# Optimization experiments

Measured on AMD Instinct MI355X. Metric: run time of the kernel, lower is better.

Reference implementation:

```python
import jax, jax.numpy as jnp
import numpy as np
import math

D_MODEL = 1024
N_HEADS = 16
D_K = D_MODEL // N_HEADS
MAX_REL = 128


def setup_inputs() -> dict:
    key = jax.random.key(0)
    ks = jax.random.split(key, 10)
    B, S = 2, 2048
    std = 1.0 / math.sqrt(D_MODEL)
    inp = {
        "x": jax.random.normal(ks[0], (B, S, D_MODEL), dtype=jnp.float32),
        "Wq": jax.random.normal(ks[1], (D_MODEL, D_MODEL), dtype=jnp.float32) * std,
        "bq": jnp.zeros((D_MODEL,), dtype=jnp.float32),
        "Wk": jax.random.normal(ks[2], (D_MODEL, D_MODEL), dtype=jnp.float32) * std,
        "bk": jnp.zeros((D_MODEL,), dtype=jnp.float32),
        "Wv": jax.random.normal(ks[3], (D_MODEL, D_MODEL), dtype=jnp.float32) * std,
        "bv": jnp.zeros((D_MODEL,), dtype=jnp.float32),
        "Wo": jax.random.normal(ks[4], (D_MODEL, D_MODEL), dtype=jnp.float32) * std,
        "bo": jnp.zeros((D_MODEL,), dtype=jnp.float32),
        "rel_bias": jax.random.normal(ks[5], (N_HEADS, 2 * MAX_REL + 1), dtype=jnp.float32) * 0.02,
    }
    return inp


def _rel_bias_matrix(rel_bias, seq_len):
    # (H, S, S) gathered relative-position bias
    pos = jnp.arange(seq_len)
    rel = pos[:, None] - pos[None, :]
    idx = jnp.clip(rel, -MAX_REL, MAX_REL) + MAX_REL  # (S, S) in [0, 2M]
    return rel_bias[:, idx]  # (H, S, S)


def reference(x, Wq, bq, Wk, bk, Wv, bv, Wo, bo, rel_bias):
    B, S, _ = x.shape
    def proj(W, b):
        y = x @ W.T + b  # torch Linear: x @ W^T + b
        return y.reshape(B, S, N_HEADS, D_K).transpose(0, 2, 1, 3)  # (B,H,S,Dk)
    Q, K, V = proj(Wq, bq), proj(Wk, bk), proj(Wv, bv)
    scores = jnp.einsum("bhqd,bhkd->bhqk", Q, K) / math.sqrt(D_K)
    scores = scores + _rel_bias_matrix(rel_bias, S)[None]
    attn = jax.nn.softmax(scores, axis=-1)
    out = jnp.einsum("bhqk,bhkd->bhqd", attn, V)
    out = out.transpose(0, 2, 1, 3).reshape(B, S, D_MODEL)
    return out @ Wo.T + bo
```

## Files before the change

kernel.cpp:

```cpp
#include <hip/hip_runtime.h>

static constexpr int DM = 1024;
static constexpr int NH = 16;
static constexpr int DK = 64;
static constexpr int S  = 2048;
static constexpr int B  = 2;
static constexpr float LOG2E = 1.4426950408889634f;
static constexpr float FMAX  = 11.0f;

typedef _Float16 f16;
typedef _Float16 f16x8 __attribute__((ext_vector_type(8)));
typedef _Float16 f16x4 __attribute__((ext_vector_type(4)));
typedef float    f32x4 __attribute__((ext_vector_type(4)));

static constexpr size_t NX = (size_t)B * S * DM;
static constexpr size_t NW = (size_t)DM * DM;

__global__ __launch_bounds__(256) void cvt_f16(const float* __restrict__ x,
                                               const float* __restrict__ wq,
                                               const float* __restrict__ wk,
                                               const float* __restrict__ wv,
                                               const float* __restrict__ wo,
                                               f16* __restrict__ xh,
                                               f16* __restrict__ wqh,
                                               f16* __restrict__ wkh,
                                               f16* __restrict__ wvh,
                                               f16* __restrict__ woh)
{
    const size_t base = ((size_t)blockIdx.x * 256 + threadIdx.x) * 8;
    const float* src; f16* dst; size_t off;
    if (base < NX) { src = x; dst = xh; off = base; }
    else {
        const size_t rem = base - NX;
        const int seg = (int)(rem >> 20);
        off = rem & (NW - 1);
        src = seg == 0 ? wq : (seg == 1 ? wk : (seg == 2 ? wv : wo));
        dst = seg == 0 ? wqh : (seg == 1 ? wkh : (seg == 2 ? wvh : woh));
    }
    float4 a = *(const float4*)&src[off];
    float4 b = *(const float4*)&src[off + 4];
    f16x8 h = { (f16)a.x, (f16)a.y, (f16)a.z, (f16)a.w,
                (f16)b.x, (f16)b.y, (f16)b.z, (f16)b.w };
    *(f16x8*)&dst[off] = h;
}

template<int MODE>
__global__ __launch_bounds__(256) void gemm_h(const f16* __restrict__ A,
                                              const f16* __restrict__ W0,
                                              const f16* __restrict__ W1,
                                              const f16* __restrict__ W2,
                                              const float* __restrict__ b0,
                                              const float* __restrict__ b1,
                                              const float* __restrict__ b2,
                                              void* __restrict__ o0,
                                              void* __restrict__ o1,
                                              void* __restrict__ o2)
{
    __shared__ f16 As[128 * 72];
    __shared__ f16 Bs[128 * 72];

    const int t    = threadIdx.x;
    const int w    = t >> 6;
    const int lane = t & 63;
    const int tx   = lane & 15;
    const int quad = lane >> 4;
    const int wm   = w >> 1;
    const int wn   = w & 1;
    const int m0   = blockIdx.y * 128;

    const f16* W; const float* bias; f16* outh = nullptr; float* outf = nullptr;
    float scale; int n0;
    if (MODE == 0) {
        const int wsel = blockIdx.x >> 3;
        n0   = (blockIdx.x & 7) * 128;
        W    = wsel == 0 ? W0 : (wsel == 1 ? W1 : W2);
        bias = wsel == 0 ? b0 : (wsel == 1 ? b1 : b2);
        outh = (f16*)(wsel == 0 ? o0 : (wsel == 1 ? o1 : o2));
        scale = wsel == 0 ? LOG2E * 0.125f : 1.0f;
    } else {
        n0 = blockIdx.x * 128;
        W = W0; bias = b0; outf = (float*)o0; scale = 1.0f;
    }

    const int lr = t >> 2;
    const int lc = (t & 3) * 8;

    f32x4 acc[4][4];
#pragma unroll
    for (int mt = 0; mt < 4; ++mt)
#pragma unroll
        for (int nt = 0; nt < 4; ++nt) acc[mt][nt] = (f32x4){0.f, 0.f, 0.f, 0.f};

    f16x8 ga[4], gb[4];
    {
        const f16* Ap = A + (size_t)(m0 + lr) * DM + lc;
        const f16* Wp = W + (size_t)(n0 + lr) * DM + lc;
        ga[0] = *(const f16x8*)(Ap);
        ga[1] = *(const f16x8*)(Ap + 32);
        ga[2] = *(const f16x8*)(Ap + (size_t)64 * DM);
        ga[3] = *(const f16x8*)(Ap + (size_t)64 * DM + 32);
        gb[0] = *(const f16x8*)(Wp);
        gb[1] = *(const f16x8*)(Wp + 32);
        gb[2] = *(const f16x8*)(Wp + (size_t)64 * DM);
        gb[3] = *(const f16x8*)(Wp + (size_t)64 * DM + 32);
    }

    for (int k0 = 0; k0 < DM; k0 += 64) {
        __syncthreads();
        *(f16x8*)&As[ lr       * 72 + lc     ] = ga[0];
        *(f16x8*)&As[ lr       * 72 + lc + 32] = ga[1];
        *(f16x8*)&As[(lr + 64) * 72 + lc     ] = ga[2];
        *(f16x8*)&As[(lr + 64) * 72 + lc + 32] = ga[3];
        *(f16x8*)&Bs[ lr       * 72 + lc     ] = gb[0];
        *(f16x8*)&Bs[ lr       * 72 + lc + 32] = gb[1];
        *(f16x8*)&Bs[(lr + 64) * 72 + lc     ] = gb[2];
        *(f16x8*)&Bs[(lr + 64) * 72 + lc + 32] = gb[3];
        if (k0 + 64 < DM) {
            const f16* Ap = A + (size_t)(m0 + lr) * DM + k0 + 64 + lc;
            const f16* Wp = W + (size_t)(n0 + lr) * DM + k0 + 64 + lc;
            ga[0] = *(const f16x8*)(Ap);
            ga[1] = *(const f16x8*)(Ap + 32);
            ga[2] = *(const f16x8*)(Ap + (size_t)64 * DM);
            ga[3] = *(const f16x8*)(Ap + (size_t)64 * DM + 32);
            gb[0] = *(const f16x8*)(Wp);
            gb[1] = *(const f16x8*)(Wp + 32);
            gb[2] = *(const f16x8*)(Wp + (size_t)64 * DM);
            gb[3] = *(const f16x8*)(Wp + (size_t)64 * DM + 32);
        }
        __syncthreads();

        f16x8 af[4][2];
#pragma unroll
        for (int mt = 0; mt < 4; ++mt)
#pragma unroll
            for (int ks = 0; ks < 2; ++ks)
                af[mt][ks] = *(const f16x8*)&As[(wm*64 + mt*16 + tx)*72 + ks*32 + quad*8];
#pragma unroll
        for (int nt = 0; nt < 4; ++nt) {
#pragma unroll
            for (int ks = 0; ks < 2; ++ks) {
                f16x8 bf = *(const f16x8*)&Bs[(wn*64 + nt*16 + tx)*72 + ks*32 + quad*8];
#pragma unroll
                for (int mt = 0; mt < 4; ++mt)
                    acc[mt][nt] = __builtin_amdgcn_mfma_f32_16x16x32_f16(af[mt][ks], bf, acc[mt][nt], 0, 0, 0);
            }
        }
    }

#pragma unroll
    for (int nt = 0; nt < 4; ++nt) {
        const int n = n0 + wn*64 + nt*16 + tx;
        const float bn = bias[n];
#pragma unroll
        for (int mt = 0; mt < 4; ++mt)
#pragma unroll
            for (int r = 0; r < 4; ++r) {
                const int m = m0 + wm*64 + mt*16 + quad*4 + r;
                const float v = (acc[mt][nt][r] + bn) * scale;
                if (MODE == 0) {
                    const int bi = m >> 11;
                    const int ss = m & (S - 1);
                    const int h  = n >> 6;
                    const int dk = n & (DK - 1);
                    outh[((size_t)((bi*NH + h)*S + ss))*DK + dk] = (f16)v;
                } else {
                    outf[(size_t)m * DM + n] = v;
                }
            }
    }
}

__global__ __launch_bounds__(256, 4) void attn_v3(const f16* __restrict__ Q,
                                                  const f16* __restrict__ K,
                                                  const f16* __restrict__ V,
                                                  const float* __restrict__ relb,
                                                  float* __restrict__ On,
                                                  float* __restrict__ lp)
{
    __shared__ f16 Ks[64*72];
    __shared__ f16 Vt[64*72];
    __shared__ float rb2[257];

    const int t    = threadIdx.x;
    const int w    = t >> 6;
    const int lane = t & 63;
    const int tx   = lane & 15;
    const int quad = lane >> 4;
    const int qt   = blockIdx.x >> 1;
    const int sp   = blockIdx.x & 1;
    const int h    = blockIdx.y;
    const int b    = blockIdx.z;
    const int q0   = qt * 128;

    const f16* Qb = Q + (size_t)((b*NH + h) * S) * DK;
    const f16* Kb = K + (size_t)((b*NH + h) * S) * DK;
    const f16* Vb = V + (size_t)((b*NH + h) * S) * DK;

    for (int i = t; i < 257; i += 256) rb2[i] = relb[h*257 + i] * LOG2E - FMAX;

    const int qrow = q0 + w*32 + tx;
    f16x8 qf[2][2];
#pragma unroll
    for (int qb = 0; qb < 2; ++qb)
#pragma unroll
        for (int ks = 0; ks < 2; ++ks)
            qf[qb][ks] = *(const f16x8*)(Qb + (size_t)(qrow + qb*16)*DK + ks*32 + quad*8);

    f32x4 oT[4][2];
    float lsum[2] = {0.f, 0.f};
#pragma unroll
    for (int d = 0; d < 4; ++d)
#pragma unroll
        for (int qb = 0; qb < 2; ++qb) oT[d][qb] = (f32x4){0.f, 0.f, 0.f, 0.f};

    const int kt0 = sp * (S/128);
    for (int kt = kt0; kt < kt0 + S/128; ++kt) {
        const int k0 = kt * 64;

        const int seq = t & 63, d0k = (t >> 6) * 16;
        f16x8 kr0 = *(const f16x8*)(Kb + (size_t)(k0 + seq)*DK + d0k);
        f16x8 kr1 = *(const f16x8*)(Kb + (size_t)(k0 + seq)*DK + d0k + 8);
        const int s2 = (t & 31) * 2, d0v = (t >> 5) * 8;
        f16x8 vr0 = *(const f16x8*)(Vb + (size_t)(k0 + s2    )*DK + d0v);
        f16x8 vr1 = *(const f16x8*)(Vb + (size_t)(k0 + s2 + 1)*DK + d0v);

        __syncthreads();
        *(f16x8*)&Ks[seq*72 + d0k    ] = kr0;
        *(f16x8*)&Ks[seq*72 + d0k + 8] = kr1;
        {
            const int g = ((s2 >> 2) & 3)*16 + (s2 >> 4)*4 + (s2 & 3);
            const unsigned short* u0 = (const unsigned short*)&vr0;
            const unsigned short* u1 = (const unsigned short*)&vr1;
#pragma unroll
            for (int j = 0; j < 8; ++j) {
                unsigned int pw = (unsigned int)u0[j] | ((unsigned int)u1[j] << 16);
                *(unsigned int*)&Vt[(d0v + j)*72 + g] = pw;
            }
        }
        __syncthreads();

        const bool farlo = (k0 - q0) >= 256;
        const bool farhi = (q0 - k0) >= 192;
        const float bconst = farlo ? rb2[0] : rb2[256];
        const int relbase = (q0 + w*32 + tx) - (k0 + quad*4);

        f16x4 pf[4][2];
#pragma unroll
        for (int sb = 0; sb < 4; ++sb) {
            f32x4 sT[2] = {(f32x4){0.f,0.f,0.f,0.f}, (f32x4){0.f,0.f,0.f,0.f}};
#pragma unroll
            for (int ks = 0; ks < 2; ++ks) {
                f16x8 kf = *(const f16x8*)&Ks[(sb*16 + tx)*72 + ks*32 + quad*8];
#pragma unroll
                for (int qb = 0; qb < 2; ++qb)
                    sT[qb] = __builtin_amdgcn_mfma_f32_16x16x32_f16(kf, qf[qb][ks], sT[qb], 0, 0, 0);
            }
            if (farlo | farhi) {
#pragma unroll
                for (int qb = 0; qb < 2; ++qb)
#pragma unroll
                    for (int r = 0; r < 4; ++r) {
                        const float p = exp2f(sT[qb][r] + bconst);
                        lsum[qb] += p;
                        pf[sb][qb][r] = (f16)p;
                    }
            } else {
#pragma unroll
                for (int qb = 0; qb < 2; ++qb)
#pragma unroll
                    for (int r = 0; r < 4; ++r) {
                        int rel = relbase + qb*16 - sb*16 - r;
                        rel = rel < -128 ? -128 : (rel > 128 ? 128 : rel);
                        const float p = exp2f(sT[qb][r] + rb2[rel + 128]);
                        lsum[qb] += p;
                        pf[sb][qb][r] = (f16)p;
                    }
            }
        }

#pragma unroll
        for (int d = 0; d < 4; ++d) {
#pragma unroll
            for (int sp2 = 0; sp2 < 2; ++sp2) {
                f16x8 vv = *(const f16x8*)&Vt[(d*16 + tx)*72 + quad*16 + sp2*8];
                f16x4 vlo = __builtin_shufflevector(vv, vv, 0, 1, 2, 3);
                f16x4 vhi = __builtin_shufflevector(vv, vv, 4, 5, 6, 7);
#pragma unroll
                for (int qb = 0; qb < 2; ++qb) {
                    oT[d][qb] = __builtin_amdgcn_mfma_f32_16x16x16f16(vlo, pf[sp2*2    ][qb], oT[d][qb], 0, 0, 0);
                    oT[d][qb] = __builtin_amdgcn_mfma_f32_16x16x16f16(vhi, pf[sp2*2 + 1][qb], oT[d][qb], 0, 0, 0);
                }
            }
        }
    }

#pragma unroll
    for (int qb = 0; qb < 2; ++qb) {
        float l = lsum[qb];
        l += __shfl_xor(l, 16);
        l += __shfl_xor(l, 32);
        const int q = q0 + w*32 + qb*16 + tx;
        if (quad == 0)
            lp[(((size_t)sp*B + b)*NH + h)*S + q] = l;
#pragma unroll
        for (int d = 0; d < 4; ++d)
            *(f32x4*)&On[(size_t)sp*NX + ((size_t)(b*S + q))*DM + h*DK + d*16 + quad*4] = oT[d][qb];
    }
}

__global__ __launch_bounds__(256) void combine(const float* __restrict__ On,
                                               const float* __restrict__ lp,
                                               f16* __restrict__ AOh)
{
    const size_t i8 = ((size_t)blockIdx.x * 256 + threadIdx.x) * 8;
    const int token = (int)(i8 >> 10);
    const int c     = (int)(i8 & (DM - 1));
    const int b     = token >> 11;
    const int st    = token & (S - 1);
    const int h     = c >> 6;
    const float l = lp[((size_t)b*NH + h)*S + st]
                  + lp[(((size_t)B + b)*NH + h)*S + st];
    const float inv = 1.0f / l;
    float4 a0 = *(const float4*)&On[i8];
    float4 a1 = *(const float4*)&On[i8 + 4];
    float4 b0 = *(const float4*)&On[NX + i8];
    float4 b1 = *(const float4*)&On[NX + i8 + 4];
    f16x8 o = { (f16)((a0.x + b0.x) * inv), (f16)((a0.y + b0.y) * inv),
                (f16)((a0.z + b0.z) * inv), (f16)((a0.w + b0.w) * inv),
                (f16)((a1.x + b1.x) * inv), (f16)((a1.y + b1.y) * inv),
                (f16)((a1.z + b1.z) * inv), (f16)((a1.w + b1.w) * inv) };
    *(f16x8*)&AOh[i8] = o;
}

extern "C" void kernel_launch(void* const* d_in, const int* in_sizes, int n_in,
                              void* d_out, int out_size, void* d_ws, size_t ws_size,
                              hipStream_t stream)
{
    const float* x    = (const float*)d_in[0];
    const float* Wq   = (const float*)d_in[1];
    const float* bq   = (const float*)d_in[2];
    const float* Wk   = (const float*)d_in[3];
    const float* bk   = (const float*)d_in[4];
    const float* Wv   = (const float*)d_in[5];
    const float* bv   = (const float*)d_in[6];
    const float* Wo   = (const float*)d_in[7];
    const float* bo   = (const float*)d_in[8];
    const float* relb = (const float*)d_in[9];

    f16* Xh  = (f16*)d_ws;
    f16* Wqh = Xh  + NX;
    f16* Wkh = Wqh + NW;
    f16* Wvh = Wkh + NW;
    f16* Woh = Wvh + NW;
    f16* Qh  = Woh + NW;
    f16* Kh  = Qh  + NX;
    f16* Vh  = Kh  + NX;
    f16* AOh = Vh  + NX;
    float* On = (float*)(AOh + NX);
    float* lpart = On + 2*NX;

    cvt_f16<<<(NX + 4*NW) / (256*8), 256, 0, stream>>>(x, Wq, Wk, Wv, Wo,
                                                       Xh, Wqh, Wkh, Wvh, Woh);
    gemm_h<0><<<dim3(24, 32), 256, 0, stream>>>(Xh, Wqh, Wkh, Wvh,
                                                bq, bk, bv, Qh, Kh, Vh);
    attn_v3<<<dim3((S/128)*2, NH, B), 256, 0, stream>>>(Qh, Kh, Vh, relb, On, lpart);
    combine<<<NX / (256*8), 256, 0, stream>>>(On, lpart, AOh);
    gemm_h<1><<<dim3(8, 32), 256, 0, stream>>>(AOh, Woh, nullptr, nullptr,
                                               bo, nullptr, nullptr,
                                               d_out, nullptr, nullptr);
}
```

Measured before the change: 219.4 us.

## Halve attention query tile, row-sum via MFMA, fold bias into accumulator, raise occupancy

The attention kernel now handles 64 queries per block (16 per wave) instead of 128 and launches twice as many blocks, with launch bounds raised to 8 blocks per CU. Row sums of the probabilities are computed by an extra MFMA against a ones vector rather than scalar adds. In far tiles the constant bias is used as the MFMA initial accumulator. The V transpose uses byte-permute instructions, and the PV MFMA section is bracketed with s_setprio. The aim is more waves to hide latency and fewer VALU ops, at the cost of K/V tiles being reloaded by twice as many blocks.

Result: slower. 247.7 us (+12.9%).

```diff
diff --git a/kernel.cpp b/kernel.cpp
--- a/kernel.cpp
+++ b/kernel.cpp
@@ -170,7 +170,7 @@
     }
 }
 
-__global__ __launch_bounds__(256, 4) void attn_v3(const f16* __restrict__ Q,
+__global__ __launch_bounds__(256, 8) void attn_v4(const f16* __restrict__ Q,
                                                   const f16* __restrict__ K,
                                                   const f16* __restrict__ V,
                                                   const float* __restrict__ relb,
@@ -190,7 +190,7 @@
     const int sp   = blockIdx.x & 1;
     const int h    = blockIdx.y;
     const int b    = blockIdx.z;
-    const int q0   = qt * 128;
+    const int q0   = qt * 64;
 
     const f16* Qb = Q + (size_t)((b*NH + h) * S) * DK;
     const f16* Kb = K + (size_t)((b*NH + h) * S) * DK;
@@ -198,20 +198,19 @@
 
     for (int i = t; i < 257; i += 256) rb2[i] = relb[h*257 + i] * LOG2E - FMAX;
 
-    const int qrow = q0 + w*32 + tx;
-    f16x8 qf[2][2];
-#pragma unroll
-    for (int qb = 0; qb < 2; ++qb)
-#pragma unroll
-        for (int ks = 0; ks < 2; ++ks)
-            qf[qb][ks] = *(const f16x8*)(Qb + (size_t)(qrow + qb*16)*DK + ks*32 + quad*8);
-
-    f32x4 oT[4][2];
-    float lsum[2] = {0.f, 0.f};
-#pragma unroll
-    for (int d = 0; d < 4; ++d)
-#pragma unroll
-        for (int qb = 0; qb < 2; ++qb) oT[d][qb] = (f32x4){0.f, 0.f, 0.f, 0.f};
+    const int qrow = q0 + w*16 + tx;
+    f16x8 qf[2];
+#pragma unroll
+    for (int ks = 0; ks < 2; ++ks)
+        qf[ks] = *(const f16x8*)(Qb + (size_t)qrow*DK + ks*32 + quad*8);
+
+    const f16 onev = (f16)(tx == 0 ? 1.0f : 0.0f);
+    const f16x4 af1 = {onev, onev, onev, onev};
+
+    f32x4 oT[4];
+    f32x4 lacc = {0.f, 0.f, 0.f, 0.f};
+#pragma unroll
+    for (int d = 0; d < 4; ++d) oT[d] = (f32x4){0.f, 0.f, 0.f, 0.f};
 
     const int kt0 = sp * (S/128);
     for (int kt = kt0; kt < kt0 + S/128; ++kt) {
@@ -229,55 +228,56 @@
         *(f16x8*)&Ks[seq*72 + d0k + 8] = kr1;
         {
             const int g = ((s2 >> 2) & 3)*16 + (s2 >> 4)*4 + (s2 & 3);
-            const unsigned short* u0 = (const unsigned short*)&vr0;
-            const unsigned short* u1 = (const unsigned short*)&vr1;
-#pragma unroll
-            for (int j = 0; j < 8; ++j) {
-                unsigned int pw = (unsigned int)u0[j] | ((unsigned int)u1[j] << 16);
-                *(unsigned int*)&Vt[(d0v + j)*72 + g] = pw;
+            const unsigned int* w0 = (const unsigned int*)&vr0;
+            const unsigned int* w1 = (const unsigned int*)&vr1;
+#pragma unroll
+            for (int jd = 0; jd < 4; ++jd) {
+                unsigned int lo = __builtin_amdgcn_perm(w1[jd], w0[jd], 0x05040100u);
+                unsigned int hi = __builtin_amdgcn_perm(w1[jd], w0[jd], 0x07060302u);
+                *(unsigned int*)&Vt[(d0v + 2*jd    )*72 + g] = lo;
+                *(unsigned int*)&Vt[(d0v + 2*jd + 1)*72 + g] = hi;
             }
         }
         __syncthreads();
 
-        const bool farlo = (k0 - q0) >= 256;
+        const bool farlo = (k0 - q0) >= 192;
         const bool farhi = (q0 - k0) >= 192;
-        const float bconst = farlo ? rb2[0] : rb2[256];
-        const int relbase = (q0 + w*32 + tx) - (k0 + quad*4);
-
-        f16x4 pf[4][2];
-#pragma unroll
-        for (int sb = 0; sb < 4; ++sb) {
-            f32x4 sT[2] = {(f32x4){0.f,0.f,0.f,0.f}, (f32x4){0.f,0.f,0.f,0.f}};
-#pragma unroll
-            for (int ks = 0; ks < 2; ++ks) {
-                f16x8 kf = *(const f16x8*)&Ks[(sb*16 + tx)*72 + ks*32 + quad*8];
-#pragma unroll
-                for (int qb = 0; qb < 2; ++qb)
-                    sT[qb] = __builtin_amdgcn_mfma_f32_16x16x32_f16(kf, qf[qb][ks], sT[qb], 0, 0, 0);
-            }
-            if (farlo | farhi) {
-#pragma unroll
-                for (int qb = 0; qb < 2; ++qb)
-#pragma unroll
-                    for (int r = 0; r < 4; ++r) {
-                        const float p = exp2f(sT[qb][r] + bconst);
-                        lsum[qb] += p;
-                        pf[sb][qb][r] = (f16)p;
-                    }
-            } else {
-#pragma unroll
-                for (int qb = 0; qb < 2; ++qb)
-#pragma unroll
-                    for (int r = 0; r < 4; ++r) {
-                        int rel = relbase + qb*16 - sb*16 - r;
-                        rel = rel < -128 ? -128 : (rel > 128 ? 128 : rel);
-                        const float p = exp2f(sT[qb][r] + rb2[rel + 128]);
-                        lsum[qb] += p;
-                        pf[sb][qb][r] = (f16)p;
-                    }
-            }
-        }
-
+
+        f16x4 pf[4];
+        if (farlo | farhi) {
+            const float bconst = farlo ? rb2[0] : rb2[256];
+            const f32x4 bc4 = {bconst, bconst, bconst, bconst};
+#pragma unroll
+            for (int sb = 0; sb < 4; ++sb) {
+                f16x8 kf0 = *(const f16x8*)&Ks[(sb*16 + tx)*72      + quad*8];
+                f16x8 kf1 = *(const f16x8*)&Ks[(sb*16 + tx)*72 + 32 + quad*8];
+                f32x4 sT = __builtin_amdgcn_mfma_f32_16x16x32_f16(kf0, qf[0], bc4, 0, 0, 0);
+                sT       = __builtin_amdgcn_mfma_f32_16x16x32_f16(kf1, qf[1], sT,  0, 0, 0);
+#pragma unroll
+                for (int r = 0; r < 4; ++r)
+                    pf[sb][r] = (f16)exp2f(sT[r]);
+                lacc = __builtin_amdgcn_mfma_f32_16x16x16f16(af1, pf[sb], lacc, 0, 0, 0);
+            }
+        } else {
+            const int relbase = qrow - (k0 + quad*4);
+            const f32x4 z4 = {0.f, 0.f, 0.f, 0.f};
+#pragma unroll
+            for (int sb = 0; sb < 4; ++sb) {
+                f16x8 kf0 = *(const f16x8*)&Ks[(sb*16 + tx)*72      + quad*8];
+                f16x8 kf1 = *(const f16x8*)&Ks[(sb*16 + tx)*72 + 32 + quad*8];
+                f32x4 sT = __builtin_amdgcn_mfma_f32_16x16x32_f16(kf0, qf[0], z4, 0, 0, 0);
+                sT       = __builtin_amdgcn_mfma_f32_16x16x32_f16(kf1, qf[1], sT, 0, 0, 0);
+#pragma unroll
+                for (int r = 0; r < 4; ++r) {
+                    int rel = relbase - sb*16 - r;
+                    rel = rel < -128 ? -128 : (rel > 128 ? 128 : rel);
+                    pf[sb][r] = (f16)exp2f(sT[r] + rb2[rel + 128]);
+                }
+                lacc = __builtin_amdgcn_mfma_f32_16x16x16f16(af1, pf[sb], lacc, 0, 0, 0);
+            }
+        }
+
+        __builtin_amdgcn_s_setprio(1);
 #pragma unroll
         for (int d = 0; d < 4; ++d) {
 #pragma unroll
@@ -285,27 +285,18 @@
                 f16x8 vv = *(const f16x8*)&Vt[(d*16 + tx)*72 + quad*16 + sp2*8];
                 f16x4 vlo = __builtin_shufflevector(vv, vv, 0, 1, 2, 3);
                 f16x4 vhi = __builtin_shufflevector(vv, vv, 4, 5, 6, 7);
-#pragma unroll
-                for (int qb = 0; qb < 2; ++qb) {
-                    oT[d][qb] = __builtin_amdgcn_mfma_f32_16x16x16f16(vlo, pf[sp2*2    ][qb], oT[d][qb], 0, 0, 0);
-                    oT[d][qb] = __builtin_amdgcn_mfma_f32_16x16x16f16(vhi, pf[sp2*2 + 1][qb], oT[d][qb], 0, 0, 0);
-                }
-            }
-        }
-    }
-
-#pragma unroll
-    for (int qb = 0; qb < 2; ++qb) {
-        float l = lsum[qb];
-        l += __shfl_xor(l, 16);
-        l += __shfl_xor(l, 32);
-        const int q = q0 + w*32 + qb*16 + tx;
-        if (quad == 0)
-            lp[(((size_t)sp*B + b)*NH + h)*S + q] = l;
-#pragma unroll
-        for (int d = 0; d < 4; ++d)
-            *(f32x4*)&On[(size_t)sp*NX + ((size_t)(b*S + q))*DM + h*DK + d*16 + quad*4] = oT[d][qb];
-    }
+                oT[d] = __builtin_amdgcn_mfma_f32_16x16x16f16(vlo, pf[sp2*2    ], oT[d], 0, 0, 0);
+                oT[d] = __builtin_amdgcn_mfma_f32_16x16x16f16(vhi, pf[sp2*2 + 1], oT[d], 0, 0, 0);
+            }
+        }
+        __builtin_amdgcn_s_setprio(0);
+    }
+
+    if (quad == 0)
+        lp[(((size_t)sp*B + b)*NH + h)*S + qrow] = lacc[0];
+#pragma unroll
+    for (int d = 0; d < 4; ++d)
+        *(f32x4*)&On[(size_t)sp*NX + ((size_t)(b*S + qrow))*DM + h*DK + d*16 + quad*4] = oT[d];
 }
 
 __global__ __launch_bounds__(256) void combine(const float* __restrict__ On,
@@ -363,7 +354,7 @@
                                                        Xh, Wqh, Wkh, Wvh, Woh);
     gemm_h<0><<<dim3(24, 32), 256, 0, stream>>>(Xh, Wqh, Wkh, Wvh,
                                                 bq, bk, bv, Qh, Kh, Vh);
-    attn_v3<<<dim3((S/128)*2, NH, B), 256, 0, stream>>>(Qh, Kh, Vh, relb, On, lpart);
+    attn_v4<<<dim3((S/64)*2, NH, B), 256, 0, stream>>>(Qh, Kh, Vh, relb, On, lpart);
     combine<<<NX / (256*8), 256, 0, stream>>>(On, lpart, AOh);
     gemm_h<1><<<dim3(8, 32), 256, 0, stream>>>(AOh, Woh, nullptr, nullptr,
                                                bo, nullptr, nullptr,
```

## Prefetch next K/V tile, compute row sums via MFMA, hoist bias branch

Applied to the files above, without the earlier changes.

Loads the next K/V tile into registers while the current tile is processed, so global load latency overlaps compute. Row sums of probabilities are accumulated with an MFMA against a ones vector instead of scalar adds and cross-lane shuffles. The constant-bias case folds the bias into the MFMA accumulator init, and the far/near branch is hoisted out of the sub-block loop. The V transpose now uses byte-permute instructions, and setprio raises priority around the PV MFMAs. The extra prefetch registers risk spills or lower occupancy.

Measured after the change: 228.1 us. +3.9%, slower.

```diff
diff --git a/kernel.cpp b/kernel.cpp
--- a/kernel.cpp
+++ b/kernel.cpp
@@ -170,7 +170,7 @@
     }
 }
 
-__global__ __launch_bounds__(256, 4) void attn_v3(const f16* __restrict__ Q,
+__global__ __launch_bounds__(256, 4) void attn_v5(const f16* __restrict__ Q,
                                                   const f16* __restrict__ K,
                                                   const f16* __restrict__ V,
                                                   const float* __restrict__ relb,
@@ -206,78 +206,100 @@
         for (int ks = 0; ks < 2; ++ks)
             qf[qb][ks] = *(const f16x8*)(Qb + (size_t)(qrow + qb*16)*DK + ks*32 + quad*8);
 
+    const f16 onev = (f16)(tx == 0 ? 1.0f : 0.0f);
+    const f16x4 af1 = {onev, onev, onev, onev};
+
     f32x4 oT[4][2];
-    float lsum[2] = {0.f, 0.f};
+    f32x4 lacc[2] = {(f32x4){0.f,0.f,0.f,0.f}, (f32x4){0.f,0.f,0.f,0.f}};
 #pragma unroll
     for (int d = 0; d < 4; ++d)
 #pragma unroll
         for (int qb = 0; qb < 2; ++qb) oT[d][qb] = (f32x4){0.f, 0.f, 0.f, 0.f};
 
+    const int seq = t & 63, d0k = (t >> 6) * 16;
+    const int s2 = (t & 31) * 2, d0v = (t >> 5) * 8;
+    const int g = ((s2 >> 2) & 3)*16 + (s2 >> 4)*4 + (s2 & 3);
+
     const int kt0 = sp * (S/128);
+    f16x8 kr0, kr1, vr0, vr1;
+    {
+        const int k0 = kt0 * 64;
+        kr0 = *(const f16x8*)(Kb + (size_t)(k0 + seq)*DK + d0k);
+        kr1 = *(const f16x8*)(Kb + (size_t)(k0 + seq)*DK + d0k + 8);
+        vr0 = *(const f16x8*)(Vb + (size_t)(k0 + s2    )*DK + d0v);
+        vr1 = *(const f16x8*)(Vb + (size_t)(k0 + s2 + 1)*DK + d0v);
+    }
+
     for (int kt = kt0; kt < kt0 + S/128; ++kt) {
         const int k0 = kt * 64;
-
-        const int seq = t & 63, d0k = (t >> 6) * 16;
-        f16x8 kr0 = *(const f16x8*)(Kb + (size_t)(k0 + seq)*DK + d0k);
-        f16x8 kr1 = *(const f16x8*)(Kb + (size_t)(k0 + seq)*DK + d0k + 8);
-        const int s2 = (t & 31) * 2, d0v = (t >> 5) * 8;
-        f16x8 vr0 = *(const f16x8*)(Vb + (size_t)(k0 + s2    )*DK + d0v);
-        f16x8 vr1 = *(const f16x8*)(Vb + (size_t)(k0 + s2 + 1)*DK + d0v);
 
         __syncthreads();
         *(f16x8*)&Ks[seq*72 + d0k    ] = kr0;
         *(f16x8*)&Ks[seq*72 + d0k + 8] = kr1;
         {
-            const int g = ((s2 >> 2) & 3)*16 + (s2 >> 4)*4 + (s2 & 3);
-            const unsigned short* u0 = (const unsigned short*)&vr0;
-            const unsigned short* u1 = (const unsigned short*)&vr1;
-#pragma unroll
-            for (int j = 0; j < 8; ++j) {
-                unsigned int pw = (unsigned int)u0[j] | ((unsigned int)u1[j] << 16);
-                *(unsigned int*)&Vt[(d0v + j)*72 + g] = pw;
-            }
+            const unsigned int* w0 = (const unsigned int*)&vr0;
+            const unsigned int* w1 = (const unsigned int*)&vr1;
+#pragma unroll
+            for (int jd = 0; jd < 4; ++jd) {
+                unsigned int pl = __builtin_amdgcn_perm(w1[jd], w0[jd], 0x05040100u);
+                unsigned int ph = __builtin_amdgcn_perm(w1[jd], w0[jd], 0x07060302u);
+                *(unsigned int*)&Vt[(d0v + 2*jd    )*72 + g] = pl;
+                *(unsigned int*)&Vt[(d0v + 2*jd + 1)*72 + g] = ph;
+            }
+        }
+        if (kt + 1 < kt0 + S/128) {
+            const int k0n = k0 + 64;
+            kr0 = *(const f16x8*)(Kb + (size_t)(k0n + seq)*DK + d0k);
+            kr1 = *(const f16x8*)(Kb + (size_t)(k0n + seq)*DK + d0k + 8);
+            vr0 = *(const f16x8*)(Vb + (size_t)(k0n + s2    )*DK + d0v);
+            vr1 = *(const f16x8*)(Vb + (size_t)(k0n + s2 + 1)*DK + d0v);
         }
         __syncthreads();
 
         const bool farlo = (k0 - q0) >= 256;
         const bool farhi = (q0 - k0) >= 192;
-        const float bconst = farlo ? rb2[0] : rb2[256];
-        const int relbase = (q0 + w*32 + tx) - (k0 + quad*4);
 
         f16x4 pf[4][2];
-#pragma unroll
-        for (int sb = 0; sb < 4; ++sb) {
-            f32x4 sT[2] = {(f32x4){0.f,0.f,0.f,0.f}, (f32x4){0.f,0.f,0.f,0.f}};
-#pragma unroll
-            for (int ks = 0; ks < 2; ++ks) {
-                f16x8 kf = *(const f16x8*)&Ks[(sb*16 + tx)*72 + ks*32 + quad*8];
-#pragma unroll
-                for (int qb = 0; qb < 2; ++qb)
-                    sT[qb] = __builtin_amdgcn_mfma_f32_16x16x32_f16(kf, qf[qb][ks], sT[qb], 0, 0, 0);
-            }
-            if (farlo | farhi) {
-#pragma unroll
-                for (int qb = 0; qb < 2; ++qb)
-#pragma unroll
-                    for (int r = 0; r < 4; ++r) {
-                        const float p = exp2f(sT[qb][r] + bconst);
-                        lsum[qb] += p;
-                        pf[sb][qb][r] = (f16)p;
-                    }
-            } else {
-#pragma unroll
-                for (int qb = 0; qb < 2; ++qb)
+        if (farlo | farhi) {
+            const float bconst = farlo ? rb2[0] : rb2[256];
+            const f32x4 bc4 = {bconst, bconst, bconst, bconst};
+#pragma unroll
+            for (int sb = 0; sb < 4; ++sb) {
+                f16x8 kf0 = *(const f16x8*)&Ks[(sb*16 + tx)*72      + quad*8];
+                f16x8 kf1 = *(const f16x8*)&Ks[(sb*16 + tx)*72 + 32 + quad*8];
+#pragma unroll
+                for (int qb = 0; qb < 2; ++qb) {
+                    f32x4 sT = __builtin_amdgcn_mfma_f32_16x16x32_f16(kf0, qf[qb][0], bc4, 0, 0, 0);
+                    sT       = __builtin_amdgcn_mfma_f32_16x16x32_f16(kf1, qf[qb][1], sT,  0, 0, 0);
+#pragma unroll
+                    for (int r = 0; r < 4; ++r)
+                        pf[sb][qb][r] = (f16)exp2f(sT[r]);
+                    lacc[qb] = __builtin_amdgcn_mfma_f32_16x16x16f16(af1, pf[sb][qb], lacc[qb], 0, 0, 0);
+                }
+            }
+        } else {
+            const int relbase = qrow - (k0 + quad*4);
+            const f32x4 z4 = {0.f, 0.f, 0.f, 0.f};
+#pragma unroll
+            for (int sb = 0; sb < 4; ++sb) {
+                f16x8 kf0 = *(const f16x8*)&Ks[(sb*16 + tx)*72      + quad*8];
+                f16x8 kf1 = *(const f16x8*)&Ks[(sb*16 + tx)*72 + 32 + quad*8];
+#pragma unroll
+                for (int qb = 0; qb < 2; ++qb) {
+                    f32x4 sT = __builtin_amdgcn_mfma_f32_16x16x32_f16(kf0, qf[qb][0], z4, 0, 0, 0);
+                    sT       = __builtin_amdgcn_mfma_f32_16x16x32_f16(kf1, qf[qb][1], sT, 0, 0, 0);
 #pragma unroll
                     for (int r = 0; r < 4; ++r) {
                         int rel = relbase + qb*16 - sb*16 - r;
                         rel = rel < -128 ? -128 : (rel > 128 ? 128 : rel);
-                        const float p = exp2f(sT[qb][r] + rb2[rel + 128]);
-                        lsum[qb] += p;
-                        pf[sb][qb][r] = (f16)p;
+                        pf[sb][qb][r] = (f16)exp2f(sT[r] + rb2[rel + 128]);
                     }
-            }
-        }
-
+                    lacc[qb] = __builtin_amdgcn_mfma_f32_16x16x16f16(af1, pf[sb][qb], lacc[qb], 0, 0, 0);
+                }
+            }
+        }
+
+        __builtin_amdgcn_s_setprio(1);
 #pragma unroll
         for (int d = 0; d < 4; ++d) {
 #pragma unroll
@@ -292,16 +314,14 @@
                 }
             }
         }
+        __builtin_amdgcn_s_setprio(0);
     }
 
 #pragma unroll
     for (int qb = 0; qb < 2; ++qb) {
-        float l = lsum[qb];
-        l += __shfl_xor(l, 16);
-        l += __shfl_xor(l, 32);
         const int q = q0 + w*32 + qb*16 + tx;
         if (quad == 0)
-            lp[(((size_t)sp*B + b)*NH + h)*S + q] = l;
+            lp[(((size_t)sp*B + b)*NH + h)*S + q] = lacc[qb][0];
 #pragma unroll
         for (int d = 0; d < 4; ++d)
             *(f32x4*)&On[(size_t)sp*NX + ((size_t)(b*S + q))*DM + h*DK + d*16 + quad*4] = oT[d][qb];
@@ -363,7 +383,7 @@
                                                        Xh, Wqh, Wkh, Wvh, Woh);
     gemm_h<0><<<dim3(24, 32), 256, 0, stream>>>(Xh, Wqh, Wkh, Wvh,
                                                 bq, bk, bv, Qh, Kh, Vh);
-    attn_v3<<<dim3((S/128)*2, NH, B), 256, 0, stream>>>(Qh, Kh, Vh, relb, On, lpart);
+    attn_v5<<<dim3((S/128)*2, NH, B), 256, 0, stream>>>(Qh, Kh, Vh, relb, On, lpart);
     combine<<<NX / (256*8), 256, 0, stream>>>(On, lpart, AOh);
     gemm_h<1><<<dim3(8, 32), 256, 0, stream>>>(AOh, Woh, nullptr, nullptr,
                                                bo, nullptr, nullptr,
```

## Stage GEMM tiles directly into LDS with global_load_lds, dropping padding

Applied to the files above, without the earlier changes.

The projection GEMM's register-staged prefetch (global to VGPR to LDS) is replaced by `__builtin_amdgcn_global_load_lds`, which writes 16-byte chunks straight into shared memory. The tiles lose their 72-element row padding so each wave's contiguous lane layout matches the unpadded 64-element rows. The aim is to cut VGPR pressure and the extra LDS store instructions. The cost is that the next tile's load is now issued only after the MFMA loop on a single buffer, so global latency no longer overlaps compute, and unpadded rows may cause LDS bank conflicts on the fragment reads.

Result: slower. 225.7 us (+2.8%).

```diff
diff --git a/kernel.cpp b/kernel.cpp
--- a/kernel.cpp
+++ b/kernel.cpp
@@ -56,8 +56,8 @@
                                               void* __restrict__ o1,
                                               void* __restrict__ o2)
 {
-    __shared__ f16 As[128 * 72];
-    __shared__ f16 Bs[128 * 72];
+    __shared__ f16 As[128 * 64];
+    __shared__ f16 Bs[128 * 64];
 
     const int t    = threadIdx.x;
     const int w    = t >> 6;
@@ -82,68 +82,54 @@
         W = W0; bias = b0; outf = (float*)o0; scale = 1.0f;
     }
 
-    const int lr = t >> 2;
-    const int lc = (t & 3) * 8;
-
     f32x4 acc[4][4];
 #pragma unroll
     for (int mt = 0; mt < 4; ++mt)
 #pragma unroll
         for (int nt = 0; nt < 4; ++nt) acc[mt][nt] = (f32x4){0.f, 0.f, 0.f, 0.f};
 
-    f16x8 ga[4], gb[4];
-    {
-        const f16* Ap = A + (size_t)(m0 + lr) * DM + lc;
-        const f16* Wp = W + (size_t)(n0 + lr) * DM + lc;
-        ga[0] = *(const f16x8*)(Ap);
-        ga[1] = *(const f16x8*)(Ap + 32);
-        ga[2] = *(const f16x8*)(Ap + (size_t)64 * DM);
-        ga[3] = *(const f16x8*)(Ap + (size_t)64 * DM + 32);
-        gb[0] = *(const f16x8*)(Wp);
-        gb[1] = *(const f16x8*)(Wp + 32);
-        gb[2] = *(const f16x8*)(Wp + (size_t)64 * DM);
-        gb[3] = *(const f16x8*)(Wp + (size_t)64 * DM + 32);
-    }
-
+    const int r8 = lane >> 3;
+    const int c8 = (lane & 7) * 8;
+    auto stage = [&](int kk) {
+        const f16* Ap = A + (size_t)(m0 + w*32 + r8) * DM + kk + c8;
+        const f16* Wp = W + (size_t)(n0 + w*32 + r8) * DM + kk + c8;
+#pragma unroll
+        for (int i = 0; i < 4; ++i) {
+            __builtin_amdgcn_global_load_lds(
+                (const __attribute__((address_space(1))) void*)(Ap + (size_t)(i*8) * DM),
+                (__attribute__((address_space(3))) void*)&As[(w*32 + i*8) * 64],
+                16, 0, 0);
+            __builtin_amdgcn_global_load_lds(
+                (const __attribute__((address_space(1))) void*)(Wp + (size_t)(i*8) * DM),
+                (__attribute__((address_space(3))) void*)&Bs[(w*32 + i*8) * 64],
+                16, 0, 0);
+        }
+    };
+
+    stage(0);
     for (int k0 = 0; k0 < DM; k0 += 64) {
         __syncthreads();
-        *(f16x8*)&As[ lr       * 72 + lc     ] = ga[0];
-        *(f16x8*)&As[ lr       * 72 + lc + 32] = ga[1];
-        *(f16x8*)&As[(lr + 64) * 72 + lc     ] = ga[2];
-        *(f16x8*)&As[(lr + 64) * 72 + lc + 32] = ga[3];
-        *(f16x8*)&Bs[ lr       * 72 + lc     ] = gb[0];
-        *(f16x8*)&Bs[ lr       * 72 + lc + 32] = gb[1];
-        *(f16x8*)&Bs[(lr + 64) * 72 + lc     ] = gb[2];
-        *(f16x8*)&Bs[(lr + 64) * 72 + lc + 32] = gb[3];
-        if (k0 + 64 < DM) {
-            const f16* Ap = A + (size_t)(m0 + lr) * DM + k0 + 64 + lc;
-            const f16* Wp = W + (size_t)(n0 + lr) * DM + k0 + 64 + lc;
-            ga[0] = *(const f16x8*)(Ap);
-            ga[1] = *(const f16x8*)(Ap + 32);
-            ga[2] = *(const f16x8*)(Ap + (size_t)64 * DM);
-            ga[3] = *(const f16x8*)(Ap + (size_t)64 * DM + 32);
-            gb[0] = *(const f16x8*)(Wp);
-            gb[1] = *(const f16x8*)(Wp + 32);
-            gb[2] = *(const f16x8*)(Wp + (size_t)64 * DM);
-            gb[3] = *(const f16x8*)(Wp + (size_t)64 * DM + 32);
-        }
-        __syncthreads();
 
         f16x8 af[4][2];
 #pragma unroll
         for (int mt = 0; mt < 4; ++mt)
 #pragma unroll
             for (int ks = 0; ks < 2; ++ks)
-                af[mt][ks] = *(const f16x8*)&As[(wm*64 + mt*16 + tx)*72 + ks*32 + quad*8];
+                af[mt][ks] = *(const f16x8*)&As[(wm*64 + mt*16 + tx)*64 + ks*32 + quad*8];
 #pragma unroll
         for (int nt = 0; nt < 4; ++nt) {
 #pragma unroll
             for (int ks = 0; ks < 2; ++ks) {
-                f16x8 bf = *(const f16x8*)&Bs[(wn*64 + nt*16 + tx)*72 + ks*32 + quad*8];
+                f16x8 bf = *(const f16x8*)&Bs[(wn*64 + nt*16 + tx)*64 + ks*32 + quad*8];
 #pragma unroll
                 for (int mt = 0; mt < 4; ++mt)
                     acc[mt][nt] = __builtin_amdgcn_mfma_f32_16x16x32_f16(af[mt][ks], bf, acc[mt][nt], 0, 0, 0);
             }
+        }
+
+        if (k0 + 64 < DM) {
+            __syncthreads();
+            stage(k0 + 64);
         }
     }
 
```
